# Kernel optimization log

Hardware: AMD Instinct MI355X
Metric: run time of the kernel (lower is better)

The kernel has to match this reference:

```python
import jax, jax.numpy as jnp
import numpy as np

D_MODEL = 2048
N_HEADS = 16
HEAD_DIM = D_MODEL // N_HEADS  # 128
HIDDEN = int(8 * D_MODEL / 3)  # 5461
EPS = 1e-6


def setup_inputs() -> dict:
    key = jax.random.key(0)
    ks = jax.random.split(key, 12)
    B, S = 2, 2048
    std = D_MODEL ** -0.5
    return {
        "x": jax.random.normal(ks[0], (B, S, D_MODEL), jnp.float32),
        "freq_cis": jax.random.normal(ks[1], (S, HEAD_DIM // 2, 2, 2), jnp.float32),
        "wq": jax.random.normal(ks[2], (D_MODEL, D_MODEL), jnp.float32) * std,
        "wk": jax.random.normal(ks[3], (D_MODEL, D_MODEL), jnp.float32) * std,
        "wv": jax.random.normal(ks[4], (D_MODEL, D_MODEL), jnp.float32) * std,
        "wo": jax.random.normal(ks[5], (D_MODEL, D_MODEL), jnp.float32) * std,
        "bo": jnp.zeros((D_MODEL,), jnp.float32),
        "w1": jax.random.normal(ks[6], (HIDDEN, D_MODEL), jnp.float32) * std,
        "w3": jax.random.normal(ks[7], (HIDDEN, D_MODEL), jnp.float32) * std,
        "w2": jax.random.normal(ks[8], (D_MODEL, HIDDEN), jnp.float32) * (HIDDEN ** -0.5),
        "g_attn": jnp.ones((D_MODEL,), jnp.float32),
        "g_ffn": jnp.ones((D_MODEL,), jnp.float32),
    }


def rmsnorm(x, g):
    xf = x.astype(jnp.float32)
    return xf * jax.lax.rsqrt(jnp.mean(xf * xf, axis=-1, keepdims=True) + EPS) * g


def rope(xq, xk, f):
    # xq/xk: [b, s, h, hd]; f: [s, hd/2, 2, 2]
    b, s, h, hd = xq.shape
    xq_ = xq.reshape(b, s, h, hd // 2, 2)
    xk_ = xk.reshape(b, s, h, hd // 2, 2)
    # out[b,s,h,i,j] = sum_k x[b,s,h,i,k] * f[s,i,j,k]
    q = jnp.einsum("bshik,sijk->bshij", xq_, f).reshape(b, s, h, hd)
    k = jnp.einsum("bshik,sijk->bshij", xk_, f).reshape(b, s, h, hd)
    return q, k


def reference(x, freq_cis, wq, wk, wv, wo, bo, w1, w3, w2, g_attn, g_ffn):
    b, s, d = x.shape
    h, hd = N_HEADS, HEAD_DIM
    scale = hd ** -0.5

    # --- attention sublayer ---
    xn = rmsnorm(x, g_attn)
    q = jnp.einsum("bsd,ed->bse", xn, wq).reshape(b, s, h, hd)
    k = jnp.einsum("bsd,ed->bse", xn, wk).reshape(b, s, h, hd)
    v = jnp.einsum("bsd,ed->bse", xn, wv).reshape(b, s, h, hd)
    q, k = rope(q, k, freq_cis[:s])
    attn = jnp.einsum("bqhd,bkhd->bhqk", q, k) * scale
    attn = jax.nn.softmax(attn, axis=-1)
    o = jnp.einsum("bhqk,bkhd->bqhd", attn, v).reshape(b, s, d)
    o = jnp.einsum("bsd,ed->bse", o, wo) + bo
    hres = x + o

    # --- SwiGLU FFN sublayer ---
    hn = rmsnorm(hres, g_ffn)
    x1 = jnp.einsum("bsd,hd->bsh", hn, w1)
    x3 = jnp.einsum("bsd,hd->bsh", hn, w3)
    ffn = jnp.einsum("bsh,dh->bsd", jax.nn.silu(x1) * x3, w2)
    return hres + ffn
```

## Files before the change

### kernel.cpp

```cpp
#include <hip/hip_runtime.h>

#define D_MODEL 2048
#define NHEADS 16
#define HDIM 128
#define HIDDEN_ 5461
#define HP2 5632
#define BATCH 2
#define SEQ 2048
#define MTOK 4096

typedef unsigned short u16;
typedef __attribute__((ext_vector_type(8))) short bf16x8;
typedef __attribute__((ext_vector_type(4))) float f32x4;
typedef __attribute__((ext_vector_type(4))) short s16x4;

__device__ __forceinline__ u16 f2b(float f) {
  union { float f; unsigned u; } v; v.f = f;
  return (u16)((v.u + 0x7FFFu + ((v.u >> 16) & 1u)) >> 16);
}
__device__ __forceinline__ float b2f(u16 u) {
  union { unsigned u; float f; } v; v.u = ((unsigned)u) << 16;
  return v.f;
}
__device__ __forceinline__ void gload16(const void* g, void* l) {
  __builtin_amdgcn_global_load_lds(
      (const __attribute__((address_space(1))) unsigned int*)g,
      (__attribute__((address_space(3))) unsigned int*)l, 16, 0, 0);
}

#define SB0() __builtin_amdgcn_sched_barrier(0)
#define BARRIER() do { SB0(); __builtin_amdgcn_s_barrier(); SB0(); } while (0)
#define LGKM0() do { asm volatile("s_waitcnt lgkmcnt(0)" ::: "memory"); SB0(); } while (0)

__global__ __launch_bounds__(256) void k_conv8(const float* __restrict__ src,
                                               u16* __restrict__ dst, int n8) {
  int stride = gridDim.x * 256;
  for (int i = blockIdx.x * 256 + threadIdx.x; i < n8; i += stride) {
    const float4* s = (const float4*)src + (size_t)i * 2;
    float4 a = s[0], b = s[1];
    bf16x8 o;
    o[0] = f2b(a.x); o[1] = f2b(a.y); o[2] = f2b(a.z); o[3] = f2b(a.w);
    o[4] = f2b(b.x); o[5] = f2b(b.y); o[6] = f2b(b.z); o[7] = f2b(b.w);
    ((bf16x8*)dst)[i] = o;
  }
}

__global__ __launch_bounds__(256) void k_conv3(const float* __restrict__ s0,
                                               const float* __restrict__ s1,
                                               const float* __restrict__ s2,
                                               u16* __restrict__ dst) {
  const int n8 = D_MODEL * D_MODEL / 8;
  int total = 3 * n8;
  int stride = gridDim.x * 256;
  for (int i = blockIdx.x * 256 + threadIdx.x; i < total; i += stride) {
    int seg = i >> 19, j = i & (n8 - 1);
    const float* s = (seg == 0) ? s0 : (seg == 1 ? s1 : s2);
    const float4* sp = (const float4*)s + (size_t)j * 2;
    float4 a = sp[0], b = sp[1];
    bf16x8 o;
    o[0] = f2b(a.x); o[1] = f2b(a.y); o[2] = f2b(a.z); o[3] = f2b(a.w);
    o[4] = f2b(b.x); o[5] = f2b(b.y); o[6] = f2b(b.z); o[7] = f2b(b.w);
    ((bf16x8*)dst)[i] = o;
  }
}

__global__ __launch_bounds__(256) void k_convpad(const float* __restrict__ src,
                                                 u16* __restrict__ dst,
                                                 int srows, int scols, int drows, int dcols) {
  size_t n = (size_t)drows * dcols;
  size_t stride = (size_t)gridDim.x * 256;
  for (size_t i = blockIdx.x * 256 + threadIdx.x; i < n; i += stride) {
    int r = (int)(i / dcols), c = (int)(i % dcols);
    float v = (r < srows && c < scols) ? src[(size_t)r * scols + c] : 0.f;
    dst[i] = f2b(v);
  }
}

__global__ __launch_bounds__(256) void k_rmsnorm(const float* __restrict__ X,
                                                 const float* __restrict__ G,
                                                 u16* __restrict__ Out) {
  int row = blockIdx.x;
  int tid = threadIdx.x;
  const float4* x4 = (const float4*)(X + (size_t)row * D_MODEL);
  float4 a = x4[tid * 2], b = x4[tid * 2 + 1];
  float ss = a.x * a.x + a.y * a.y + a.z * a.z + a.w * a.w +
             b.x * b.x + b.y * b.y + b.z * b.z + b.w * b.w;
#pragma unroll
  for (int off = 1; off < 64; off <<= 1) ss += __shfl_xor(ss, off);
  __shared__ float part[4];
  if ((tid & 63) == 0) part[tid >> 6] = ss;
  __syncthreads();
  float rstd = rsqrtf((part[0] + part[1] + part[2] + part[3]) * (1.0f / D_MODEL) + 1e-6f);
  const float4* g4 = (const float4*)G;
  float4 ga = g4[tid * 2], gb = g4[tid * 2 + 1];
  bf16x8 o;
  o[0] = f2b(a.x * rstd * ga.x); o[1] = f2b(a.y * rstd * ga.y);
  o[2] = f2b(a.z * rstd * ga.z); o[3] = f2b(a.w * rstd * ga.w);
  o[4] = f2b(b.x * rstd * gb.x); o[5] = f2b(b.y * rstd * gb.y);
  o[6] = f2b(b.z * rstd * gb.z); o[7] = f2b(b.w * rstd * gb.w);
  *((bf16x8*)(Out + (size_t)row * D_MODEL) + tid) = o;
}

template <int WN, int EPI>
__global__ __launch_bounds__(512, 2) void k_gemm2(const u16* __restrict__ A,
                                                  const u16* __restrict__ Bw,
                                                  void* __restrict__ O0,
                                                  void* __restrict__ O1,
                                                  void* __restrict__ O2,
                                                  const float* __restrict__ bias,
                                                  const float* __restrict__ res,
                                                  const u16* __restrict__ aux,
                                                  int M, int N, int K) {
  constexpr int BN = WN * 64;
  constexpr int PB = BN * 64;
  __shared__ __align__(128) char lds[65536 + 4 * PB];
  const int tid = threadIdx.x;
  const int w = tid >> 6, lane = tid & 63;
  const int lo = lane & 15, hi = lane >> 4;
  const int wr = w >> 2, wc = w & 3;

  const int ntN = N / BN;
  const int nwg = gridDim.x * gridDim.y;
  const int flat = blockIdx.y * gridDim.x + blockIdx.x;
  const int swz = (flat & 7) * (nwg >> 3) + (flat >> 3);
  const int tm = swz / ntN, tn = swz % ntN;
  const int m0 = tm * 256, n0 = tn * BN;

  auto stA = [&](int nb, int kk, int k0) {
#pragma unroll
    for (int j = 0; j < 2; ++j) {
      int row = j * 128 + (tid >> 2);
      const u16* g = A + (size_t)(m0 + row) * K + k0 + kk * 32 + (tid & 3) * 8;
      gload16(g, lds + nb * 32768 + kk * 16384 + j * 8192 + tid * 16);
    }
  };
  auto stB = [&](int nb, int kk, int k0) {
#pragma unroll
    for (int j = 0; j < WN / 2; ++j) {
      int row = j * 128 + (tid >> 2);
      const u16* g = Bw + (size_t)(n0 + row) * K + k0 + kk * 32 + (tid & 3) * 8;
      gload16(g, lds + 65536 + nb * 2 * PB + kk * PB + j * 8192 + tid * 16);
    }
  };
  auto ldA = [&](int buf, int kk, int mf) {
    return *(const bf16x8*)(lds + buf * 32768 + kk * 16384 +
                            (wr * 128 + mf * 16 + lo) * 64 + hi * 16);
  };
  auto ldB = [&](int buf, int kk, int nf) {
    return *(const bf16x8*)(lds + 65536 + buf * 2 * PB + kk * PB +
                            (wc * (WN * 16) + nf * 16 + lo) * 64 + hi * 16);
  };
#define VMCNT_CONFIRM()                                             \
  do {                                                              \
    if constexpr (WN == 4)                                          \
      asm volatile("s_waitcnt vmcnt(4)" ::: "memory");              \
    else                                                            \
      asm volatile("s_waitcnt vmcnt(3)" ::: "memory");              \
    SB0();                                                          \
  } while (0)

  f32x4 acc[8][WN];
#pragma unroll
  for (int i = 0; i < 8; i++)
#pragma unroll
    for (int j = 0; j < WN; j++) acc[i][j] = (f32x4){0.f, 0.f, 0.f, 0.f};

  stA(0, 0, 0);
  stB(0, 0, 0);
  stA(0, 1, 0);
  stB(0, 1, 0);
  VMCNT_CONFIRM();
  BARRIER();

  const int KT = K / 64;
  for (int kt = 0; kt < KT; ++kt) {
    const int buf = kt & 1, nb = buf ^ 1;
    int kn = (kt + 1) * 64;
    if (kn >= K) kn = 0;
    bf16x8 aF[4], bF[WN];

#pragma unroll
    for (int i = 0; i < 4; i++) aF[i] = ldA(buf, 0, i);
#pragma unroll
    for (int j = 0; j < WN; j++) bF[j] = ldB(buf, 0, j);
    stA(nb, 0, kn);
    BARRIER();
    LGKM0();
    __builtin_amdgcn_s_setprio(1);
#pragma unroll
    for (int i = 0; i < 4; i++)
#pragma unroll
      for (int j = 0; j < WN; j++)
        acc[i][j] = __builtin_amdgcn_mfma_f32_16x16x32_bf16(aF[i], bF[j], acc[i][j], 0, 0, 0);
    __builtin_amdgcn_s_setprio(0);
    BARRIER();

#pragma unroll
    for (int i = 0; i < 4; i++) aF[i] = ldA(buf, 0, 4 + i);
    stB(nb, 0, kn);
    VMCNT_CONFIRM();
    BARRIER();
    LGKM0();
    __builtin_amdgcn_s_setprio(1);
#pragma unroll
    for (int i = 0; i < 4; i++)
#pragma unroll
      for (int j = 0; j < WN; j++)
        acc[4 + i][j] = __builtin_amdgcn_mfma_f32_16x16x32_bf16(aF[i], bF[j], acc[4 + i][j], 0, 0, 0);
    __builtin_amdgcn_s_setprio(0);
    BARRIER();

#pragma unroll
    for (int i = 0; i < 4; i++) aF[i] = ldA(buf, 1, i);
#pragma unroll
    for (int j = 0; j < WN; j++) bF[j] = ldB(buf, 1, j);
    stA(nb, 1, kn);
    BARRIER();
    LGKM0();
    __builtin_amdgcn_s_setprio(1);
#pragma unroll
    for (int i = 0; i < 4; i++)
#pragma unroll
      for (int j = 0; j < WN; j++)
        acc[i][j] = __builtin_amdgcn_mfma_f32_16x16x32_bf16(aF[i], bF[j], acc[i][j], 0, 0, 0);
    __builtin_amdgcn_s_setprio(0);
    BARRIER();

#pragma unroll
    for (int i = 0; i < 4; i++) aF[i] = ldA(buf, 1, 4 + i);
    stB(nb, 1, kn);
    VMCNT_CONFIRM();
    BARRIER();
    LGKM0();
    __builtin_amdgcn_s_setprio(1);
#pragma unroll
    for (int i = 0; i < 4; i++)
#pragma unroll
      for (int j = 0; j < WN; j++)
        acc[4 + i][j] = __builtin_amdgcn_mfma_f32_16x16x32_bf16(aF[i], bF[j], acc[4 + i][j], 0, 0, 0);
    __builtin_amdgcn_s_setprio(0);
    BARRIER();
  }

  u16* qkvout = nullptr;
  int c0 = 0;
  if (EPI == 1) {
    int seg = n0 >> 11;
    qkvout = (u16*)(seg == 0 ? O0 : (seg == 1 ? O1 : O2));
    c0 = n0 & 2047;
  }
#pragma unroll
  for (int i = 0; i < 8; i++) {
#pragma unroll
    for (int j = 0; j < WN; j++) {
      int colL = wc * (WN * 16) + j * 16 + lo;
#pragma unroll
      for (int r = 0; r < 4; r++) {
        int row = m0 + wr * 128 + i * 16 + hi * 4 + r;
        float v = acc[i][j][r];
        if (EPI == 0) {
          ((u16*)O0)[(size_t)row * N + n0 + colL] = f2b(v);
        } else if (EPI == 1) {
          qkvout[(size_t)row * 2048 + c0 + colL] = f2b(v);
        } else if (EPI == 2) {
          size_t idx = (size_t)row * N + n0 + colL;
          ((float*)O0)[idx] = v + bias[n0 + colL] + res[idx];
        } else if (EPI == 3) {
          size_t idx = (size_t)row * N + n0 + colL;
          ((float*)O0)[idx] = v + res[idx];
        } else {
          size_t idx = (size_t)row * N + n0 + colL;
          float v1 = b2f(aux[idx]);
          float sig = 1.f / (1.f + __expf(-v1));
          ((u16*)O0)[idx] = f2b(v1 * sig * v);
        }
      }
    }
  }
#undef VMCNT_CONFIRM
}

__global__ __launch_bounds__(256) void k_rope(u16* __restrict__ Qb, u16* __restrict__ Kb,
                                              const float* __restrict__ F) {
  int n = MTOK * (D_MODEL / 2);
  int stride = gridDim.x * 256;
  for (int t = blockIdx.x * 256 + threadIdx.x; t < n; t += stride) {
    int i = t & 63;
    int rest = t >> 6;
    int hh = rest & 15;
    int tok = rest >> 4;
    int s = tok & (SEQ - 1);
    float4 f = ((const float4*)F)[s * 64 + i];
    size_t off = (size_t)tok * D_MODEL + hh * HDIM + i * 2;
    float x0 = b2f(Qb[off]), x1 = b2f(Qb[off + 1]);
    Qb[off] = f2b(x0 * f.x + x1 * f.y);
    Qb[off + 1] = f2b(x0 * f.z + x1 * f.w);
    x0 = b2f(Kb[off]); x1 = b2f(Kb[off + 1]);
    Kb[off] = f2b(x0 * f.x + x1 * f.y);
    Kb[off + 1] = f2b(x0 * f.z + x1 * f.w);
  }
}

__global__ __launch_bounds__(256) void k_vt(const u16* __restrict__ V, u16* __restrict__ VT) {
  __shared__ u16 t[64][72];
  const int stile = blockIdx.x;
  const int bh = blockIdx.y;
  const int dz = blockIdx.z;
  const int b = bh >> 4, h = bh & 15;
  const int tok0 = b * SEQ + stile * 64;
  const int d0 = dz * 64;
  const int tid = threadIdx.x;
#pragma unroll
  for (int p = 0; p < 2; p++) {
    int idx = p * 256 + tid;
    int row = idx >> 3, seg = idx & 7;
    bf16x8 v = *(const bf16x8*)(V + (size_t)(tok0 + row) * D_MODEL + h * HDIM + d0 + seg * 8);
    *(bf16x8*)(&t[row][seg * 8]) = v;
  }
  __syncthreads();
#pragma unroll
  for (int p = 0; p < 2; p++) {
    int idx = p * 256 + tid;
    int dr = idx >> 3, seg = idx & 7;
    bf16x8 o;
#pragma unroll
    for (int e = 0; e < 8; e++) o[e] = t[seg * 8 + e][dr];
    *(bf16x8*)(VT + ((size_t)bh * HDIM + d0 + dr) * SEQ + stile * 64 + seg * 8) = o;
  }
}

__global__ __launch_bounds__(256) void k_flash3(const u16* __restrict__ Q,
                                                const u16* __restrict__ Kb,
                                                const u16* __restrict__ VT,
                                                u16* __restrict__ O) {
  __shared__ u16 Kt[64 * 128];
  __shared__ u16 Vt[128 * 64];
  __shared__ u16 Pl[4][2][16 * 72];
  const int tid = threadIdx.x;
  const int w = tid >> 6, lane = tid & 63;
  const int lo = lane & 15, hi = lane >> 4;
  const int qt = blockIdx.x, bh = blockIdx.y;
  const int b = bh >> 4, h = bh & 15;
  const size_t qrow0 = (size_t)b * SEQ + qt * 128 + w * 32;
  const float SC = 0.08838834764831845f * 1.4426950408889634f;

  bf16x8 aQ[2][4];
#pragma unroll
  for (int qg = 0; qg < 2; qg++)
#pragma unroll
    for (int kb = 0; kb < 4; kb++)
      aQ[qg][kb] = *(const bf16x8*)(Q + (qrow0 + qg * 16 + lo) * D_MODEL + h * HDIM + kb * 32 + hi * 8);

  float m_s[2] = {-3.0e38f, -3.0e38f}, l_s[2] = {0.f, 0.f};
  f32x4 oacc[2][8];
#pragma unroll
  for (int qg = 0; qg < 2; qg++)
#pragma unroll
    for (int d = 0; d < 8; d++) oacc[qg][d] = (f32x4){0.f, 0.f, 0.f, 0.f};

  const int krowL = tid >> 4;
  const int kslot = (tid & 15) ^ (krowL & 7);
  const int vrowL = tid >> 3;
  const int vslot = (tid & 7) ^ (vrowL & 7);
  const u16* Kbase = Kb + (size_t)b * SEQ * D_MODEL + h * HDIM;
  const u16* Vbase = VT + (size_t)bh * HDIM * SEQ;
  unsigned* Plw = (unsigned*)&Pl[w][0][0];

  for (int kt = 0; kt < SEQ / 64; kt++) {
    __syncthreads();
#pragma unroll
    for (int t = 0; t < 4; t++) {
      int row = t * 16 + krowL;
      const u16* g = Kbase + (size_t)(kt * 64 + row) * D_MODEL + kslot * 8;
      gload16(g, (char*)Kt + t * 4096 + tid * 16);
    }
#pragma unroll
    for (int t = 0; t < 4; t++) {
      int row = t * 32 + vrowL;
      const u16* g = Vbase + (size_t)row * SEQ + kt * 64 + vslot * 8;
      gload16(g, (char*)Vt + t * 4096 + tid * 16);
    }
    __syncthreads();

    f32x4 sf[2][4];
#pragma unroll
    for (int cb = 0; cb < 4; cb++) {
      bf16x8 kA[4];
#pragma unroll
      for (int kb = 0; kb < 4; kb++) {
        int ps = (kb * 4 + hi) ^ (lo & 7);
        kA[kb] = *(const bf16x8*)(Kt + (cb * 16 + lo) * 128 + ps * 8);
      }
#pragma unroll
      for (int qg = 0; qg < 2; qg++) {
        f32x4 s = (f32x4){0.f, 0.f, 0.f, 0.f};
#pragma unroll
        for (int kb = 0; kb < 4; kb++)
          s = __builtin_amdgcn_mfma_f32_16x16x32_bf16(kA[kb], aQ[qg][kb], s, 0, 0, 0);
        sf[qg][cb] = s;
      }
    }

    float tsc[2];
    bool ok = true;
#pragma unroll
    for (int qg = 0; qg < 2; qg++) {
      float t0 = fmaxf(fmaxf(sf[qg][0][0], sf[qg][0][1]), fmaxf(sf[qg][0][2], sf[qg][0][3]));
      float t1 = fmaxf(fmaxf(sf[qg][1][0], sf[qg][1][1]), fmaxf(sf[qg][1][2], sf[qg][1][3]));
      float t2 = fmaxf(fmaxf(sf[qg][2][0], sf[qg][2][1]), fmaxf(sf[qg][2][2], sf[qg][2][3]));
      float t3 = fmaxf(fmaxf(sf[qg][3][0], sf[qg][3][1]), fmaxf(sf[qg][3][2], sf[qg][3][3]));
      float t = fmaxf(fmaxf(t0, t1), fmaxf(t2, t3));
      t = fmaxf(t, __shfl_xor(t, 16));
      t = fmaxf(t, __shfl_xor(t, 32));
      tsc[qg] = t * SC;
      ok = ok && (tsc[qg] - m_s[qg] <= 11.5f);
    }
    bool skip = __all(ok);
#pragma unroll
    for (int qg = 0; qg < 2; qg++) {
      float mm = m_s[qg];
      if (!skip) {
        mm = fmaxf(m_s[qg], tsc[qg]);
        float alpha = exp2f(m_s[qg] - mm);
        l_s[qg] *= alpha;
#pragma unroll
        for (int d = 0; d < 8; d++) oacc[qg][d] *= alpha;
        m_s[qg] = mm;
      }
      float rs = 0.f;
#pragma unroll
      for (int cb = 0; cb < 4; cb++) {
        float p0 = exp2f(sf[qg][cb][0] * SC - mm);
        float p1 = exp2f(sf[qg][cb][1] * SC - mm);
        float p2 = exp2f(sf[qg][cb][2] * SC - mm);
        float p3 = exp2f(sf[qg][cb][3] * SC - mm);
        rs += (p0 + p1) + (p2 + p3);
        unsigned pk0, pk1;
        asm("v_cvt_pk_bf16_f32 %0, %1, %2" : "=v"(pk0) : "v"(p0), "v"(p1));
        asm("v_cvt_pk_bf16_f32 %0, %1, %2" : "=v"(pk1) : "v"(p2), "v"(p3));
        Plw[qg * 576 + lo * 36 + cb * 8 + hi * 2 + 0] = pk0;
        Plw[qg * 576 + lo * 36 + cb * 8 + hi * 2 + 1] = pk1;
      }
      rs += __shfl_xor(rs, 16);
      rs += __shfl_xor(rs, 32);
      l_s[qg] += rs;
    }
    LGKM0();

    bf16x8 aP[2][2];
#pragma unroll
    for (int qg = 0; qg < 2; qg++)
#pragma unroll
      for (int ks = 0; ks < 2; ks++)
        aP[qg][ks] = *(const bf16x8*)(&Pl[w][qg][lo * 72 + ks * 32 + hi * 8]);
#pragma unroll
    for (int db = 0; db < 8; db++) {
      bf16x8 vA[2];
#pragma unroll
      for (int ks = 0; ks < 2; ks++) {
        int ps = (ks * 4 + hi) ^ (lo & 7);
        vA[ks] = *(const bf16x8*)(Vt + (db * 16 + lo) * 64 + ps * 8);
      }
#pragma unroll
      for (int qg = 0; qg < 2; qg++)
#pragma unroll
        for (int ks = 0; ks < 2; ks++)
          oacc[qg][db] = __builtin_amdgcn_mfma_f32_16x16x32_bf16(vA[ks], aP[qg][ks], oacc[qg][db], 0, 0, 0);
    }
  }

#pragma unroll
  for (int qg = 0; qg < 2; qg++) {
    float inv = 1.f / l_s[qg];
    size_t rowoff = (qrow0 + qg * 16 + lo) * D_MODEL + h * HDIM;
#pragma unroll
    for (int db = 0; db < 8; db++) {
      s16x4 o;
#pragma unroll
      for (int r = 0; r < 4; r++) o[r] = (short)f2b(oacc[qg][db][r] * inv);
      *(s16x4*)(O + rowoff + db * 16 + hi * 4) = o;
    }
  }
}

extern "C" void kernel_launch(void* const* d_in, const int* in_sizes, int n_in,
                              void* d_out, int out_size, void* d_ws, size_t ws_size,
                              hipStream_t stream) {
  (void)in_sizes; (void)n_in; (void)out_size; (void)ws_size;
  const float* x  = (const float*)d_in[0];
  const float* fc = (const float*)d_in[1];
  const float* wq = (const float*)d_in[2];
  const float* wk = (const float*)d_in[3];
  const float* wv = (const float*)d_in[4];
  const float* wo = (const float*)d_in[5];
  const float* bo = (const float*)d_in[6];
  const float* w1 = (const float*)d_in[7];
  const float* w3 = (const float*)d_in[8];
  const float* w2 = (const float*)d_in[9];
  const float* ga = (const float*)d_in[10];
  const float* gf = (const float*)d_in[11];
  float* out = (float*)d_out;

  char* p = (char*)d_ws;
  auto alloc = [&](size_t bytes) { char* r = p; p += (bytes + 255) & ~(size_t)255; return r; };
  u16* xn  = (u16*)alloc((size_t)MTOK * D_MODEL * 2);
  u16* qb  = (u16*)alloc((size_t)MTOK * D_MODEL * 2);
  u16* kb  = (u16*)alloc((size_t)MTOK * D_MODEL * 2);
  u16* vb  = (u16*)alloc((size_t)MTOK * D_MODEL * 2);
  u16* x1  = (u16*)alloc((size_t)MTOK * HP2 * 2);
  u16* wsl = (u16*)alloc((size_t)3 * D_MODEL * D_MODEL * 2);
  u16* vbt = xn;
  u16* ob  = vb;
  u16* hn  = qb;

  k_rmsnorm<<<MTOK, 256, 0, stream>>>(x, ga, xn);
  k_conv3<<<1536, 256, 0, stream>>>(wq, wk, wv, wsl);
  k_gemm2<2, 1><<<dim3(6144 / 128, MTOK / 256), 512, 0, stream>>>(
      xn, wsl, qb, kb, vb, nullptr, nullptr, nullptr, MTOK, 6144, D_MODEL);
  k_rope<<<1024, 256, 0, stream>>>(qb, kb, fc);
  k_vt<<<dim3(SEQ / 64, BATCH * NHEADS, 2), 256, 0, stream>>>(vb, vbt);
  dim3 gfl(SEQ / 128, BATCH * NHEADS);
  k_flash3<<<gfl, 256, 0, stream>>>(qb, kb, vbt, ob);
  k_conv8<<<1024, 256, 0, stream>>>(wo, wsl, D_MODEL * D_MODEL / 8);
  k_gemm2<2, 2><<<dim3(2048 / 128, MTOK / 256), 512, 0, stream>>>(
      ob, wsl, out, nullptr, nullptr, bo, x, nullptr, MTOK, D_MODEL, D_MODEL);

  k_rmsnorm<<<MTOK, 256, 0, stream>>>(out, gf, hn);
  k_convpad<<<1024, 256, 0, stream>>>(w1, wsl, HIDDEN_, D_MODEL, HP2, D_MODEL);
  k_gemm2<2, 0><<<dim3(HP2 / 128, MTOK / 256), 512, 0, stream>>>(
      hn, wsl, x1, nullptr, nullptr, nullptr, nullptr, nullptr, MTOK, HP2, D_MODEL);
  k_convpad<<<1024, 256, 0, stream>>>(w3, wsl, HIDDEN_, D_MODEL, HP2, D_MODEL);
  k_gemm2<2, 4><<<dim3(HP2 / 128, MTOK / 256), 512, 0, stream>>>(
      hn, wsl, x1, nullptr, nullptr, nullptr, nullptr, x1, MTOK, HP2, D_MODEL);
  k_convpad<<<1024, 256, 0, stream>>>(w2, wsl, D_MODEL, HIDDEN_, D_MODEL, HP2);
  k_gemm2<2, 3><<<dim3(2048 / 128, MTOK / 256), 512, 0, stream>>>(
      x1, wsl, out, nullptr, nullptr, nullptr, out, nullptr, MTOK, D_MODEL, HP2);
}
```

Baseline: 819.3 us.

## Double-buffer K/V tiles in flash attention and widen GEMM N-tiles

The flash attention kernel now double-buffers its K and V shared-memory tiles. It issues async global-to-LDS loads for the next tile before computing the current one, using a partial vmcnt wait and one barrier per iteration. The P staging buffer is cut to one per wave and reused per query group, with extra LGKM waits. Separately, the QKV and W1/W3 GEMMs move to a wider template tile (4 instead of 2) with half as many column blocks. Together these aim to overlap memory latency with compute and raise GEMM operand reuse, at the cost of doubled LDS for K/V and possibly lower occupancy.

```diff
diff --git a/kernel.cpp b/kernel.cpp
--- a/kernel.cpp
+++ b/kernel.cpp
@@ -329,13 +329,13 @@
   }
 }
 
-__global__ __launch_bounds__(256) void k_flash3(const u16* __restrict__ Q,
+__global__ __launch_bounds__(256) void k_flash5(const u16* __restrict__ Q,
                                                 const u16* __restrict__ Kb,
                                                 const u16* __restrict__ VT,
                                                 u16* __restrict__ O) {
-  __shared__ u16 Kt[64 * 128];
-  __shared__ u16 Vt[128 * 64];
-  __shared__ u16 Pl[4][2][16 * 72];
+  __shared__ u16 Kt[2][64 * 128];
+  __shared__ u16 Vt[2][128 * 64];
+  __shared__ u16 Pl[4][16 * 72];
   const int tid = threadIdx.x;
   const int w = tid >> 6, lane = tid & 63;
   const int lo = lane & 15, hi = lane >> 4;
@@ -364,23 +364,37 @@
   const int vslot = (tid & 7) ^ (vrowL & 7);
   const u16* Kbase = Kb + (size_t)b * SEQ * D_MODEL + h * HDIM;
   const u16* Vbase = VT + (size_t)bh * HDIM * SEQ;
-  unsigned* Plw = (unsigned*)&Pl[w][0][0];
-
-  for (int kt = 0; kt < SEQ / 64; kt++) {
-    __syncthreads();
+  unsigned* Plw = (unsigned*)&Pl[w][0];
+
+  auto stage = [&](int bb, int kt) {
 #pragma unroll
     for (int t = 0; t < 4; t++) {
       int row = t * 16 + krowL;
-      const u16* g = Kbase + (size_t)(kt * 64 + row) * D_MODEL + kslot * 8;
-      gload16(g, (char*)Kt + t * 4096 + tid * 16);
+      gload16(Kbase + (size_t)(kt * 64 + row) * D_MODEL + kslot * 8,
+              (char*)&Kt[bb][0] + t * 4096 + tid * 16);
     }
 #pragma unroll
     for (int t = 0; t < 4; t++) {
       int row = t * 32 + vrowL;
-      const u16* g = Vbase + (size_t)row * SEQ + kt * 64 + vslot * 8;
-      gload16(g, (char*)Vt + t * 4096 + tid * 16);
-    }
-    __syncthreads();
+      gload16(Vbase + (size_t)row * SEQ + kt * 64 + vslot * 8,
+              (char*)&Vt[bb][0] + t * 4096 + tid * 16);
+    }
+  };
+
+  stage(0, 0);
+  const int NT = SEQ / 64;
+  for (int kt = 0; kt < NT; kt++) {
+    const int cur = kt & 1;
+    if (kt + 1 < NT) {
+      stage(cur ^ 1, kt + 1);
+      asm volatile("s_waitcnt vmcnt(8)" ::: "memory");
+    } else {
+      asm volatile("s_waitcnt vmcnt(0)" ::: "memory");
+    }
+    SB0();
+    BARRIER();
+    const u16* KtC = &Kt[cur][0];
+    const u16* VtC = &Vt[cur][0];
 
     f32x4 sf[2][4];
 #pragma unroll
@@ -389,7 +403,7 @@
 #pragma unroll
       for (int kb = 0; kb < 4; kb++) {
         int ps = (kb * 4 + hi) ^ (lo & 7);
-        kA[kb] = *(const bf16x8*)(Kt + (cb * 16 + lo) * 128 + ps * 8);
+        kA[kb] = *(const bf16x8*)(KtC + (cb * 16 + lo) * 128 + ps * 8);
       }
 #pragma unroll
       for (int qg = 0; qg < 2; qg++) {
@@ -416,6 +430,8 @@
       ok = ok && (tsc[qg] - m_s[qg] <= 11.5f);
     }
     bool skip = __all(ok);
+
+    bf16x8 aP[2][2];
 #pragma unroll
     for (int qg = 0; qg < 2; qg++) {
       float mm = m_s[qg];
@@ -438,28 +454,25 @@
         unsigned pk0, pk1;
         asm("v_cvt_pk_bf16_f32 %0, %1, %2" : "=v"(pk0) : "v"(p0), "v"(p1));
         asm("v_cvt_pk_bf16_f32 %0, %1, %2" : "=v"(pk1) : "v"(p2), "v"(p3));
-        Plw[qg * 576 + lo * 36 + cb * 8 + hi * 2 + 0] = pk0;
-        Plw[qg * 576 + lo * 36 + cb * 8 + hi * 2 + 1] = pk1;
+        Plw[lo * 36 + cb * 8 + hi * 2 + 0] = pk0;
+        Plw[lo * 36 + cb * 8 + hi * 2 + 1] = pk1;
       }
       rs += __shfl_xor(rs, 16);
       rs += __shfl_xor(rs, 32);
       l_s[qg] += rs;
-    }
-    LGKM0();
-
-    bf16x8 aP[2][2];
-#pragma unroll
-    for (int qg = 0; qg < 2; qg++)
-#pragma unroll
-      for (int ks = 0; ks < 2; ks++)
-        aP[qg][ks] = *(const bf16x8*)(&Pl[w][qg][lo * 72 + ks * 32 + hi * 8]);
+      LGKM0();
+      aP[qg][0] = *(const bf16x8*)(&Pl[w][lo * 72 + 0 * 32 + hi * 8]);
+      aP[qg][1] = *(const bf16x8*)(&Pl[w][lo * 72 + 1 * 32 + hi * 8]);
+      LGKM0();
+    }
+
 #pragma unroll
     for (int db = 0; db < 8; db++) {
       bf16x8 vA[2];
 #pragma unroll
       for (int ks = 0; ks < 2; ks++) {
         int ps = (ks * 4 + hi) ^ (lo & 7);
-        vA[ks] = *(const bf16x8*)(Vt + (db * 16 + lo) * 64 + ps * 8);
+        vA[ks] = *(const bf16x8*)(VtC + (db * 16 + lo) * 64 + ps * 8);
       }
 #pragma unroll
       for (int qg = 0; qg < 2; qg++)
@@ -467,6 +480,7 @@
         for (int ks = 0; ks < 2; ks++)
           oacc[qg][db] = __builtin_amdgcn_mfma_f32_16x16x32_bf16(vA[ks], aP[qg][ks], oacc[qg][db], 0, 0, 0);
     }
+    BARRIER();
   }
 
 #pragma unroll
@@ -515,22 +529,22 @@
 
   k_rmsnorm<<<MTOK, 256, 0, stream>>>(x, ga, xn);
   k_conv3<<<1536, 256, 0, stream>>>(wq, wk, wv, wsl);
-  k_gemm2<2, 1><<<dim3(6144 / 128, MTOK / 256), 512, 0, stream>>>(
+  k_gemm2<4, 1><<<dim3(6144 / 256, MTOK / 256), 512, 0, stream>>>(
       xn, wsl, qb, kb, vb, nullptr, nullptr, nullptr, MTOK, 6144, D_MODEL);
   k_rope<<<1024, 256, 0, stream>>>(qb, kb, fc);
   k_vt<<<dim3(SEQ / 64, BATCH * NHEADS, 2), 256, 0, stream>>>(vb, vbt);
   dim3 gfl(SEQ / 128, BATCH * NHEADS);
-  k_flash3<<<gfl, 256, 0, stream>>>(qb, kb, vbt, ob);
+  k_flash5<<<gfl, 256, 0, stream>>>(qb, kb, vbt, ob);
   k_conv8<<<1024, 256, 0, stream>>>(wo, wsl, D_MODEL * D_MODEL / 8);
   k_gemm2<2, 2><<<dim3(2048 / 128, MTOK / 256), 512, 0, stream>>>(
       ob, wsl, out, nullptr, nullptr, bo, x, nullptr, MTOK, D_MODEL, D_MODEL);
 
   k_rmsnorm<<<MTOK, 256, 0, stream>>>(out, gf, hn);
   k_convpad<<<1024, 256, 0, stream>>>(w1, wsl, HIDDEN_, D_MODEL, HP2, D_MODEL);
-  k_gemm2<2, 0><<<dim3(HP2 / 128, MTOK / 256), 512, 0, stream>>>(
+  k_gemm2<4, 0><<<dim3(HP2 / 256, MTOK / 256), 512, 0, stream>>>(
       hn, wsl, x1, nullptr, nullptr, nullptr, nullptr, nullptr, MTOK, HP2, D_MODEL);
   k_convpad<<<1024, 256, 0, stream>>>(w3, wsl, HIDDEN_, D_MODEL, HP2, D_MODEL);
-  k_gemm2<2, 4><<<dim3(HP2 / 128, MTOK / 256), 512, 0, stream>>>(
+  k_gemm2<4, 4><<<dim3(HP2 / 256, MTOK / 256), 512, 0, stream>>>(
       hn, wsl, x1, nullptr, nullptr, nullptr, nullptr, x1, MTOK, HP2, D_MODEL);
   k_convpad<<<1024, 256, 0, stream>>>(w2, wsl, D_MODEL, HIDDEN_, D_MODEL, HP2);
   k_gemm2<2, 3><<<dim3(2048 / 128, MTOK / 256), 512, 0, stream>>>(
```

Result: slower. 837.8 us (+2.3%).

## Merge W1/W3 GEMMs into one wide launch and vectorize weight conversion

Applied to the files above, without the earlier changes.

The FFN up-projections are merged into a single GEMM over N=11264. Each tile selects the w1 or w3 bf16 weight buffer and writes its result to x1 or x3. The SiLU-gate product moves out of the GEMM epilogue into a separate elementwise kernel. The scalar, div/mod-based padded conversion for w1/w3 is replaced by a vectorized row-contiguous converter. The QKV and merged GEMMs switch to the wider WN=4 tile. The change cuts launches and conversion overhead, at the cost of an extra x3 buffer and an additional read/write pass over the hidden activations; the padded w3 copy reuses the kb/vb region.

```diff
diff --git a/kernel.cpp b/kernel.cpp
--- a/kernel.cpp
+++ b/kernel.cpp
@@ -64,6 +64,24 @@
   }
 }
 
+__global__ __launch_bounds__(256) void k_convrows(const float* __restrict__ src,
+                                                  u16* __restrict__ dst,
+                                                  int n8src, int n8dst) {
+  int stride = gridDim.x * 256;
+  for (int i = blockIdx.x * 256 + threadIdx.x; i < n8dst; i += stride) {
+    bf16x8 o;
+    if (i < n8src) {
+      const float4* sp = (const float4*)src + (size_t)i * 2;
+      float4 a = sp[0], b = sp[1];
+      o[0] = f2b(a.x); o[1] = f2b(a.y); o[2] = f2b(a.z); o[3] = f2b(a.w);
+      o[4] = f2b(b.x); o[5] = f2b(b.y); o[6] = f2b(b.z); o[7] = f2b(b.w);
+    } else {
+      o = (bf16x8){0, 0, 0, 0, 0, 0, 0, 0};
+    }
+    ((bf16x8*)dst)[i] = o;
+  }
+}
+
 __global__ __launch_bounds__(256) void k_convpad(const float* __restrict__ src,
                                                  u16* __restrict__ dst,
                                                  int srows, int scols, int drows, int dcols) {
@@ -73,6 +91,24 @@
     int r = (int)(i / dcols), c = (int)(i % dcols);
     float v = (r < srows && c < scols) ? src[(size_t)r * scols + c] : 0.f;
     dst[i] = f2b(v);
+  }
+}
+
+__global__ __launch_bounds__(256) void k_silumul(u16* __restrict__ X1,
+                                                 const u16* __restrict__ X3, int n8) {
+  int stride = gridDim.x * 256;
+  for (int i = blockIdx.x * 256 + threadIdx.x; i < n8; i += stride) {
+    bf16x8 a = ((const bf16x8*)X1)[i];
+    bf16x8 b = ((const bf16x8*)X3)[i];
+    bf16x8 o;
+#pragma unroll
+    for (int e = 0; e < 8; e++) {
+      float v1 = b2f((u16)a[e]);
+      float v3 = b2f((u16)b[e]);
+      float sig = 1.f / (1.f + __expf(-v1));
+      o[e] = f2b(v1 * sig * v3);
+    }
+    ((bf16x8*)X1)[i] = o;
   }
 }
 
@@ -104,6 +140,7 @@
 template <int WN, int EPI>
 __global__ __launch_bounds__(512, 2) void k_gemm2(const u16* __restrict__ A,
                                                   const u16* __restrict__ Bw,
+                                                  const u16* __restrict__ Bw2,
                                                   void* __restrict__ O0,
                                                   void* __restrict__ O1,
                                                   void* __restrict__ O2,
@@ -126,6 +163,12 @@
   const int tm = swz / ntN, tn = swz % ntN;
   const int m0 = tm * 256, n0 = tn * BN;
 
+  const u16* bbase;
+  if (EPI == 5)
+    bbase = (n0 < 5632) ? Bw + (size_t)n0 * K : Bw2 + (size_t)(n0 - 5632) * K;
+  else
+    bbase = Bw + (size_t)n0 * K;
+
   auto stA = [&](int nb, int kk, int k0) {
 #pragma unroll
     for (int j = 0; j < 2; ++j) {
@@ -138,7 +181,7 @@
 #pragma unroll
     for (int j = 0; j < WN / 2; ++j) {
       int row = j * 128 + (tid >> 2);
-      const u16* g = Bw + (size_t)(n0 + row) * K + k0 + kk * 32 + (tid & 3) * 8;
+      const u16* g = bbase + (size_t)row * K + k0 + kk * 32 + (tid & 3) * 8;
       gload16(g, lds + 65536 + nb * 2 * PB + kk * PB + j * 8192 + tid * 16);
     }
   };
@@ -249,6 +292,12 @@
     qkvout = (u16*)(seg == 0 ? O0 : (seg == 1 ? O1 : O2));
     c0 = n0 & 2047;
   }
+  u16* w13out = nullptr;
+  int w13c0 = 0;
+  if (EPI == 5) {
+    w13out = (u16*)(n0 < 5632 ? O0 : O1);
+    w13c0 = (n0 < 5632) ? n0 : n0 - 5632;
+  }
 #pragma unroll
   for (int i = 0; i < 8; i++) {
 #pragma unroll
@@ -268,11 +317,13 @@
         } else if (EPI == 3) {
           size_t idx = (size_t)row * N + n0 + colL;
           ((float*)O0)[idx] = v + res[idx];
-        } else {
+        } else if (EPI == 4) {
           size_t idx = (size_t)row * N + n0 + colL;
           float v1 = b2f(aux[idx]);
           float sig = 1.f / (1.f + __expf(-v1));
           ((u16*)O0)[idx] = f2b(v1 * sig * v);
+        } else {
+          w13out[(size_t)row * 5632 + w13c0 + colL] = f2b(v);
         }
       }
     }
@@ -508,31 +559,32 @@
   u16* kb  = (u16*)alloc((size_t)MTOK * D_MODEL * 2);
   u16* vb  = (u16*)alloc((size_t)MTOK * D_MODEL * 2);
   u16* x1  = (u16*)alloc((size_t)MTOK * HP2 * 2);
+  u16* x3  = (u16*)alloc((size_t)MTOK * HP2 * 2);
   u16* wsl = (u16*)alloc((size_t)3 * D_MODEL * D_MODEL * 2);
   u16* vbt = xn;
   u16* ob  = vb;
   u16* hn  = qb;
+  u16* w3b = kb;
 
   k_rmsnorm<<<MTOK, 256, 0, stream>>>(x, ga, xn);
   k_conv3<<<1536, 256, 0, stream>>>(wq, wk, wv, wsl);
-  k_gemm2<2, 1><<<dim3(6144 / 128, MTOK / 256), 512, 0, stream>>>(
-      xn, wsl, qb, kb, vb, nullptr, nullptr, nullptr, MTOK, 6144, D_MODEL);
+  k_gemm2<4, 1><<<dim3(6144 / 256, MTOK / 256), 512, 0, stream>>>(
+      xn, wsl, nullptr, qb, kb, vb, nullptr, nullptr, nullptr, MTOK, 6144, D_MODEL);
   k_rope<<<1024, 256, 0, stream>>>(qb, kb, fc);
   k_vt<<<dim3(SEQ / 64, BATCH * NHEADS, 2), 256, 0, stream>>>(vb, vbt);
   dim3 gfl(SEQ / 128, BATCH * NHEADS);
   k_flash3<<<gfl, 256, 0, stream>>>(qb, kb, vbt, ob);
   k_conv8<<<1024, 256, 0, stream>>>(wo, wsl, D_MODEL * D_MODEL / 8);
   k_gemm2<2, 2><<<dim3(2048 / 128, MTOK / 256), 512, 0, stream>>>(
-      ob, wsl, out, nullptr, nullptr, bo, x, nullptr, MTOK, D_MODEL, D_MODEL);
+      ob, wsl, nullptr, out, nullptr, nullptr, bo, x, nullptr, MTOK, D_MODEL, D_MODEL);
 
   k_rmsnorm<<<MTOK, 256, 0, stream>>>(out, gf, hn);
-  k_convpad<<<1024, 256, 0, stream>>>(w1, wsl, HIDDEN_, D_MODEL, HP2, D_MODEL);
-  k_gemm2<2, 0><<<dim3(HP2 / 128, MTOK / 256), 512, 0, stream>>>(
-      hn, wsl, x1, nullptr, nullptr, nullptr, nullptr, nullptr, MTOK, HP2, D_MODEL);
-  k_convpad<<<1024, 256, 0, stream>>>(w3, wsl, HIDDEN_, D_MODEL, HP2, D_MODEL);
-  k_gemm2<2, 4><<<dim3(HP2 / 128, MTOK / 256), 512, 0, stream>>>(
-      hn, wsl, x1, nullptr, nullptr, nullptr, nullptr, x1, MTOK, HP2, D_MODEL);
+  k_convrows<<<1024, 256, 0, stream>>>(w1, wsl, HIDDEN_ * D_MODEL / 8, HP2 * D_MODEL / 8);
+  k_convrows<<<1024, 256, 0, stream>>>(w3, w3b, HIDDEN_ * D_MODEL / 8, HP2 * D_MODEL / 8);
+  k_gemm2<4, 5><<<dim3(11264 / 256, MTOK / 256), 512, 0, stream>>>(
+      hn, wsl, w3b, x1, x3, nullptr, nullptr, nullptr, nullptr, MTOK, 11264, D_MODEL);
+  k_silumul<<<2048, 256, 0, stream>>>(x1, x3, MTOK * HP2 / 8);
   k_convpad<<<1024, 256, 0, stream>>>(w2, wsl, D_MODEL, HIDDEN_, D_MODEL, HP2);
   k_gemm2<2, 3><<<dim3(2048 / 128, MTOK / 256), 512, 0, stream>>>(
-      x1, wsl, out, nullptr, nullptr, nullptr, out, nullptr, MTOK, D_MODEL, HP2);
-}
+      x1, wsl, nullptr, out, nullptr, nullptr, nullptr, out, nullptr, MTOK, D_MODEL, HP2);
+}
```

Measured after the change: 753.6 us. -8.0%, faster.
